# Optimization experiments

Measured on AMD Instinct MI355X. Metric: run time of the kernel, lower is better.

Reference implementation:

```python
import jax, jax.numpy as jnp
import numpy as np

N_NODE = 100000
N_EDGE = 1600000
D_FEAT = 64
DEPTH = 3
BASEALPHA = 1.0


def setup_inputs() -> dict:
    key = jax.random.key(0)
    k1, k2, k3 = jax.random.split(key, 3)
    x = jax.random.normal(k1, (N_NODE, D_FEAT), dtype=jnp.float32)
    edge_index = jax.random.randint(k2, (2, N_EDGE), 0, N_NODE, dtype=jnp.int64)
    edge_attr = jax.random.uniform(k3, (N_EDGE,), dtype=jnp.float32)
    # learnable polynomial coefficients, init = min(1/alpha, 1) = 1.0
    alphas = jnp.ones((DEPTH + 1,), dtype=jnp.float32)
    return {"x": x, "edge_index": edge_index, "edge_attr": edge_attr, "alphas": alphas}


def reference(x, edge_index, edge_attr, alphas):
    n = x.shape[0]
    row, col = edge_index[0], edge_index[1]
    # GCN symmetric degree normalization: val_e = d_row^-1/2 * w_e * d_col^-1/2
    deg = jax.ops.segment_sum(edge_attr, row, num_segments=n)
    safe_deg = jnp.where(deg > 0, deg, 1.0)
    dinv = jnp.where(deg > 0, jax.lax.rsqrt(safe_deg), 0.0)
    val = dinv[row] * edge_attr * dinv[col]  # [E]

    a = BASEALPHA * jnp.tanh(alphas)  # [depth+1]

    def spmm(h):  # (adj @ h): out[i] = sum_{e: row_e=i} val_e * h[col_e]
        return jax.ops.segment_sum(val[:, None] * h[col], row, num_segments=n)

    # PowerConv recurrence: x_0 = x; x_L = a_L * (adj @ x_{L-1})
    xs = [x]
    for L in range(1, DEPTH + 1):
        xs.append(a[L] * spmm(xs[-1]))
    return jnp.stack(xs, axis=1)  # [N, depth+1, d]
```

## Files before the change

kernel.cpp:

```cpp
#include <hip/hip_runtime.h>
#include <math.h>

#define N_NODE 100000
#define N_EDGE 1600000
#define D_FEAT 64
#define DEPTH  3
#define OUT_STRIDE ((DEPTH + 1) * D_FEAT)

#define NB  256
#define RPB 391
#define CAP 8192
#define S1_BS 512
#define S1_CHUNK 8192
#define S1_BLOCKS ((N_EDGE + S1_CHUNK - 1) / S1_CHUNK)

#define NOCT 16
#define OCT_DIV 6250
#define NCELL (RPB * NOCT)
#define NCHUNK (NCELL / 8)

#define DEG_SCALE 33554432.0f

typedef float  f32x4 __attribute__((ext_vector_type(4)));

__device__ __forceinline__ unsigned int bf16_rne(float f) {
    unsigned int u = __float_as_uint(f);
    return (u + 0x7FFFu + ((u >> 16) & 1u)) >> 16;
}

__global__ __launch_bounds__(S1_BS) void stage1_bucket(
        const int* __restrict__ ei, const float* __restrict__ ea,
        int* __restrict__ bucket_cursor, int2* __restrict__ bucket) {
    __shared__ int hist[NB];
    __shared__ int segb[NB];
    int tid = threadIdx.x;
    int e0 = blockIdx.x * S1_CHUNK;

    for (int i = tid; i < NB; i += S1_BS) hist[i] = 0;
    __syncthreads();

    for (int k = 0; k < S1_CHUNK; k += S1_BS) {
        int e = e0 + k + tid;
        if (e < N_EDGE) {
            int r = ei[e];
            atomicAdd(&hist[r / RPB], 1);
        }
    }
    __syncthreads();

    for (int i = tid; i < NB; i += S1_BS) {
        int h = hist[i];
        segb[i] = (h > 0) ? atomicAdd(&bucket_cursor[i], h) : 0;
        hist[i] = 0;
    }
    __syncthreads();

    for (int k = 0; k < S1_CHUNK; k += S1_BS) {
        int e = e0 + k + tid;
        if (e < N_EDGE) {
            int r  = ei[e];
            int b  = r / RPB;
            int rl = r - b * RPB;
            int c  = ei[N_EDGE + e];
            float w = ea[e];
            int lofs = atomicAdd(&hist[b], 1);
            int pos  = segb[b] + lofs;
            if (pos < CAP)
                bucket[(size_t)b * CAP + pos] =
                    make_int2((rl << 17) | c, __float_as_int(w));
        }
    }
}

__global__ void bucket_scan_kernel(const int* __restrict__ bucket_cursor,
                                   int* __restrict__ bucket_base,
                                   const float* __restrict__ alphas,
                                   float* __restrict__ a_vals) {
    __shared__ int sc[NB];
    int tid = threadIdx.x;
    int v = bucket_cursor[tid];
    sc[tid] = v;
    __syncthreads();
    for (int off = 1; off < NB; off <<= 1) {
        int t = (tid >= off) ? sc[tid - off] : 0;
        __syncthreads();
        sc[tid] += t;
        __syncthreads();
    }
    bucket_base[tid] = sc[tid] - v;
    if (tid < DEPTH + 1) a_vals[tid] = tanhf(alphas[tid]);
}

__global__ __launch_bounds__(1024) void stage2_fused(
        const int2* __restrict__ bucket, const int* __restrict__ bucket_cnt,
        const int* __restrict__ bucket_base,
        int* __restrict__ row_ptr, int* __restrict__ row_end,
        float* __restrict__ dinv, int2* __restrict__ csr) {
    __shared__ int          cnt2[NCELL];
    __shared__ unsigned int wdeg[RPB];
    __shared__ int          sc[1024];
    __shared__ int2         staged[CAP];
    int b = blockIdx.x, tid = threadIdx.x;

    for (int i = tid; i < NCELL; i += 1024) cnt2[i] = 0;
    if (tid < RPB) wdeg[tid] = 0u;
    __syncthreads();

    int cnt = bucket_cnt[b];
    const int2* src = bucket + (size_t)b * CAP;

    for (int i = tid; i < cnt; i += 1024) {
        int2 e = src[i];
        int rl = e.x >> 17;
        int c  = e.x & 0x1FFFF;
        int oc = c / OCT_DIV;
        atomicAdd(&cnt2[rl * NOCT + oc], 1);
        atomicAdd(&wdeg[rl],
                  (unsigned int)(__int_as_float(e.y) * DEG_SCALE + 0.5f));
    }
    __syncthreads();

    int lsum = 0;
    if (tid < NCHUNK) {
        int base = tid * 8;
        #pragma unroll
        for (int j = 0; j < 8; ++j) lsum += cnt2[base + j];
    }
    sc[tid] = lsum;
    __syncthreads();
    for (int off = 1; off < 1024; off <<= 1) {
        int t = (tid >= off) ? sc[tid - off] : 0;
        __syncthreads();
        sc[tid] += t;
        __syncthreads();
    }
    if (tid < NCHUNK) {
        int run = sc[tid] - lsum;
        int base = tid * 8;
        #pragma unroll
        for (int j = 0; j < 8; ++j) {
            int v = cnt2[base + j];
            cnt2[base + j] = run;
            run += v;
        }
    }
    __syncthreads();

    int base_b = bucket_base[b];
    if (tid < RPB) {
        int row = b * RPB + tid;
        if (row < N_NODE) {
            int rb = cnt2[tid * NOCT];
            int re = (tid == RPB - 1) ? cnt : cnt2[(tid + 1) * NOCT];
            row_ptr[row] = base_b + rb;
            row_end[row] = base_b + re;
            float d = (float)wdeg[tid] * (1.0f / DEG_SCALE);
            dinv[row] = (d > 0.0f) ? rsqrtf(d) : 0.0f;
        }
    }
    __syncthreads();

    for (int i = tid; i < cnt; i += 1024) {
        int2 e = src[i];
        int rl = e.x >> 17;
        int c  = e.x & 0x1FFFF;
        int oc = c / OCT_DIV;
        int pos = atomicAdd(&cnt2[rl * NOCT + oc], 1);
        staged[pos] = make_int2(c, e.y);
    }
    __syncthreads();

    for (int i = tid; i < cnt; i += 1024) csr[base_b + i] = staged[i];
}

__global__ void init_out_kernel(const float* __restrict__ x,
                                const float* __restrict__ dinv,
                                float* __restrict__ out,
                                unsigned short* __restrict__ hb0,
                                int write_hb) {
    int i = blockIdx.x * blockDim.x + threadIdx.x;
    if (i < N_NODE * (D_FEAT / 4)) {
        int n  = i >> 4;
        int d4 = (i & 15) << 2;
        float4 v = *(const float4*)&x[(size_t)n * D_FEAT + d4];
        f32x4 vv = {v.x, v.y, v.z, v.w};
        __builtin_nontemporal_store(
            vv, (f32x4*)&out[(size_t)n * OUT_STRIDE + d4]);
        if (write_hb) {
            float s = dinv[n];
            uint2 o;
            o.x = bf16_rne(v.x * s) | (bf16_rne(v.y * s) << 16);
            o.y = bf16_rne(v.z * s) | (bf16_rne(v.w * s) << 16);
            *(uint2*)&hb0[(size_t)n * D_FEAT + d4] = o;
        }
    }
}

__global__ __launch_bounds__(256) void spmm_bf16_kernel(
        const int* __restrict__ row_ptr,
        const int* __restrict__ row_end,
        const int2* __restrict__ csr,
        const float* __restrict__ a_vals,
        const float* __restrict__ dinv,
        const unsigned short* __restrict__ hsrc,
        unsigned short* __restrict__ hdst,
        float* __restrict__ out,
        int L, int write_hdst) {
    int node = blockIdx.x * (blockDim.x >> 6) + (threadIdx.x >> 6);
    int lane = threadIdx.x & 63;
    if (node >= N_NODE) return;
    int beg = row_ptr[node];
    int end = row_end[node];
    int g = lane >> 3;
    int q = lane & 7;

    float acc[8] = {0, 0, 0, 0, 0, 0, 0, 0};

    for (int chunk = beg; chunk < end; chunk += 64) {
        int idx = chunk + lane;
        int2 pv = (idx < end) ? csr[idx] : make_int2(0, 0);
        int navail = end - chunk;
        if (navail > 64) navail = 64;
        for (int t = 0; t < navail; t += 8) {
            int sub = t + g;
            int   cc = __shfl(pv.x, sub);
            float vv = __int_as_float(__shfl(pv.y, sub));
            bool valid = (sub < navail);
            int   c_safe = valid ? cc : 0;
            float v_safe = valid ? vv : 0.0f;
            uint4 hv = *(const uint4*)&hsrc[(size_t)c_safe * D_FEAT + (q << 3)];
            acc[0] += v_safe * __uint_as_float((hv.x & 0xFFFFu) << 16);
            acc[1] += v_safe * __uint_as_float(hv.x & 0xFFFF0000u);
            acc[2] += v_safe * __uint_as_float((hv.y & 0xFFFFu) << 16);
            acc[3] += v_safe * __uint_as_float(hv.y & 0xFFFF0000u);
            acc[4] += v_safe * __uint_as_float((hv.z & 0xFFFFu) << 16);
            acc[5] += v_safe * __uint_as_float(hv.z & 0xFFFF0000u);
            acc[6] += v_safe * __uint_as_float((hv.w & 0xFFFFu) << 16);
            acc[7] += v_safe * __uint_as_float(hv.w & 0xFFFF0000u);
        }
    }

    #pragma unroll
    for (int j = 0; j < 8; ++j) {
        acc[j] += __shfl_down(acc[j], 32);
        acc[j] += __shfl_down(acc[j], 16);
        acc[j] += __shfl_down(acc[j], 8);
    }

    if (g == 0) {
        float di = dinv[node];
        float aL = a_vals[L];
        float s1 = aL * di;
        float s2 = s1 * di;
        f32x4 r0 = {s1 * acc[0], s1 * acc[1], s1 * acc[2], s1 * acc[3]};
        f32x4 r1 = {s1 * acc[4], s1 * acc[5], s1 * acc[6], s1 * acc[7]};
        size_t ob = (size_t)node * OUT_STRIDE + L * D_FEAT + (q << 3);
        __builtin_nontemporal_store(r0, (f32x4*)&out[ob]);
        __builtin_nontemporal_store(r1, (f32x4*)&out[ob + 4]);
        if (write_hdst) {
            uint4 o;
            o.x = bf16_rne(s2 * acc[0]) | (bf16_rne(s2 * acc[1]) << 16);
            o.y = bf16_rne(s2 * acc[2]) | (bf16_rne(s2 * acc[3]) << 16);
            o.z = bf16_rne(s2 * acc[4]) | (bf16_rne(s2 * acc[5]) << 16);
            o.w = bf16_rne(s2 * acc[6]) | (bf16_rne(s2 * acc[7]) << 16);
            *(uint4*)&hdst[(size_t)node * D_FEAT + (q << 3)] = o;
        }
    }
}

__global__ void spmm_f32_kernel(const int* __restrict__ row_ptr,
                                const int* __restrict__ row_end,
                                const int2* __restrict__ csr,
                                const float* __restrict__ a_vals,
                                const float* __restrict__ dinv,
                                float* __restrict__ out,
                                int L) {
    int node = blockIdx.x * (blockDim.x >> 6) + (threadIdx.x >> 6);
    int lane = threadIdx.x & 63;
    if (node >= N_NODE) return;
    int beg = row_ptr[node];
    int end = row_end[node];
    int g = lane >> 4;
    int q = lane & 15;
    int src_base = (L - 1) * D_FEAT + (q << 2);

    float4 acc = make_float4(0.0f, 0.0f, 0.0f, 0.0f);
    for (int chunk = beg; chunk < end; chunk += 64) {
        int idx = chunk + lane;
        int2 pv = (idx < end) ? csr[idx] : make_int2(0, 0);
        int navail = end - chunk;
        if (navail > 64) navail = 64;
        for (int t = 0; t < navail; t += 4) {
            int sub = t + g;
            int   cc = __shfl(pv.x, sub);
            float vv = __int_as_float(__shfl(pv.y, sub));
            bool valid = (sub < navail);
            int   c_safe = valid ? cc : 0;
            float v_safe = valid ? (vv * dinv[c_safe]) : 0.0f;
            const float4 hv =
                *(const float4*)&out[(size_t)c_safe * OUT_STRIDE + src_base];
            acc.x += v_safe * hv.x;
            acc.y += v_safe * hv.y;
            acc.z += v_safe * hv.z;
            acc.w += v_safe * hv.w;
        }
    }
    acc.x += __shfl_down(acc.x, 32);
    acc.y += __shfl_down(acc.y, 32);
    acc.z += __shfl_down(acc.z, 32);
    acc.w += __shfl_down(acc.w, 32);
    acc.x += __shfl_down(acc.x, 16);
    acc.y += __shfl_down(acc.y, 16);
    acc.z += __shfl_down(acc.z, 16);
    acc.w += __shfl_down(acc.w, 16);
    if (g == 0) {
        float s1 = a_vals[L] * dinv[node];
        float4 r = make_float4(s1 * acc.x, s1 * acc.y, s1 * acc.z, s1 * acc.w);
        *(float4*)&out[(size_t)node * OUT_STRIDE + L * D_FEAT + (q << 2)] = r;
    }
}

extern "C" void kernel_launch(void* const* d_in, const int* in_sizes, int n_in,
                              void* d_out, int out_size, void* d_ws, size_t ws_size,
                              hipStream_t stream) {
    const float* x      = (const float*)d_in[0];
    const int*   ei     = (const int*)d_in[1];
    const float* ea     = (const float*)d_in[2];
    const float* alphas = (const float*)d_in[3];
    float*       out    = (float*)d_out;

    int2*  csr          = (int2*)d_ws;
    int*   row_ptr      = (int*)(csr + N_EDGE);
    int*   row_end      = row_ptr + N_NODE;
    float* dinv         = (float*)(row_end + N_NODE);
    int*   bucket_cursor= (int*)(dinv + N_NODE);
    int*   bucket_base  = bucket_cursor + NB;
    float* a_vals       = (float*)(bucket_base + NB);
    int2*  bucket       = (int2*)(a_vals + 4);
    unsigned short* hb0 = (unsigned short*)bucket;
    unsigned short* hb1 = hb0 + (size_t)N_NODE * D_FEAT;

    size_t base_bytes = (size_t)((char*)bucket - (char*)d_ws);
    size_t need_bf16  = base_bytes +
        2 * (size_t)N_NODE * D_FEAT * sizeof(unsigned short);
    int use_bf16 = (ws_size >= need_bf16) ? 1 : 0;

    hipMemsetAsync(bucket_cursor, 0, NB * sizeof(int), stream);

    stage1_bucket<<<S1_BLOCKS, S1_BS, 0, stream>>>(ei, ea, bucket_cursor, bucket);
    bucket_scan_kernel<<<1, NB, 0, stream>>>(bucket_cursor, bucket_base,
                                             alphas, a_vals);
    stage2_fused<<<NB, 1024, 0, stream>>>(bucket, bucket_cursor, bucket_base,
                                          row_ptr, row_end, dinv, csr);
    init_out_kernel<<<(N_NODE * (D_FEAT / 4) + 255) / 256, 256, 0, stream>>>(
        x, dinv, out, hb0, use_bf16);

    int nodes_per_block = 256 / 64;
    int spmm_blocks = (N_NODE + nodes_per_block - 1) / nodes_per_block;
    if (use_bf16) {
        spmm_bf16_kernel<<<spmm_blocks, 256, 0, stream>>>(row_ptr, row_end, csr,
            a_vals, dinv, hb0, hb1, out, 1, 1);
        spmm_bf16_kernel<<<spmm_blocks, 256, 0, stream>>>(row_ptr, row_end, csr,
            a_vals, dinv, hb1, hb0, out, 2, 1);
        spmm_bf16_kernel<<<spmm_blocks, 256, 0, stream>>>(row_ptr, row_end, csr,
            a_vals, dinv, hb0, hb1, out, 3, 0);
    } else {
        for (int L = 1; L <= DEPTH; ++L) {
            spmm_f32_kernel<<<spmm_blocks, 256, 0, stream>>>(row_ptr, row_end, csr,
                a_vals, dinv, out, L);
        }
    }
}
```

Before: 331.3 us.

## Split bf16 feature buffer into 16-feature slabs processed in separate passes

The bf16 hidden-state buffer is re-laid out as four slabs of 16 features each, and the SpMM kernel runs one pass per slab, with 16 lanes per node instead of 64. Each pass gathers from a 3.2 MB slab that can stay resident in cache, so random neighbour gathers hit cache instead of HBM. The cost is reading the CSR edge list four times per layer and doing more launch-level work per node. CSR loads are also made nontemporal.

```diff
diff --git a/kernel.cpp b/kernel.cpp
--- a/kernel.cpp
+++ b/kernel.cpp
@@ -18,6 +18,11 @@
 #define OCT_DIV 6250
 #define NCELL (RPB * NOCT)
 #define NCHUNK (NCELL / 8)
+
+#define PASSES 4
+#define FPP    16
+#define NODES_PER_BLOCK 16
+#define BPP (N_NODE / NODES_PER_BLOCK)
 
 #define DEG_SCALE 33554432.0f
 
@@ -188,10 +193,12 @@
             vv, (f32x4*)&out[(size_t)n * OUT_STRIDE + d4]);
         if (write_hb) {
             float s = dinv[n];
+            int pass = d4 >> 4;
+            int fo   = d4 & 15;
             uint2 o;
             o.x = bf16_rne(v.x * s) | (bf16_rne(v.y * s) << 16);
             o.y = bf16_rne(v.z * s) | (bf16_rne(v.w * s) << 16);
-            *(uint2*)&hb0[(size_t)n * D_FEAT + d4] = o;
+            *(uint2*)&hb0[((size_t)pass * N_NODE + n) * FPP + fo] = o;
         }
     }
 }
@@ -206,29 +213,40 @@
         unsigned short* __restrict__ hdst,
         float* __restrict__ out,
         int L, int write_hdst) {
-    int node = blockIdx.x * (blockDim.x >> 6) + (threadIdx.x >> 6);
+    int pass = blockIdx.x / BPP;
+    int nb   = blockIdx.x - pass * BPP;
     int lane = threadIdx.x & 63;
-    if (node >= N_NODE) return;
+    int grp  = lane >> 4;
+    int node = nb * NODES_PER_BLOCK + (threadIdx.x >> 6) * 4 + grp;
+    int l16  = lane & 15;
+    int s    = l16 >> 1;
+    int f    = l16 & 1;
+
     int beg = row_ptr[node];
     int end = row_end[node];
-    int g = lane >> 3;
-    int q = lane & 7;
+
+    const unsigned short* slab = hsrc + (size_t)pass * N_NODE * FPP;
 
     float acc[8] = {0, 0, 0, 0, 0, 0, 0, 0};
 
-    for (int chunk = beg; chunk < end; chunk += 64) {
-        int idx = chunk + lane;
-        int2 pv = (idx < end) ? csr[idx] : make_int2(0, 0);
+    for (int chunk = beg; chunk < end; chunk += 16) {
+        int idx = chunk + l16;
+        int2 pv = make_int2(0, 0);
+        if (idx < end) {
+            long long t =
+                __builtin_nontemporal_load((const long long*)(csr + idx));
+            pv = *(int2*)&t;
+        }
         int navail = end - chunk;
-        if (navail > 64) navail = 64;
+        if (navail > 16) navail = 16;
         for (int t = 0; t < navail; t += 8) {
-            int sub = t + g;
-            int   cc = __shfl(pv.x, sub);
-            float vv = __int_as_float(__shfl(pv.y, sub));
+            int sub = t + s;
+            int   cc = __shfl(pv.x, sub, 16);
+            float vv = __int_as_float(__shfl(pv.y, sub, 16));
             bool valid = (sub < navail);
             int   c_safe = valid ? cc : 0;
             float v_safe = valid ? vv : 0.0f;
-            uint4 hv = *(const uint4*)&hsrc[(size_t)c_safe * D_FEAT + (q << 3)];
+            uint4 hv = *(const uint4*)&slab[(size_t)c_safe * FPP + (f << 3)];
             acc[0] += v_safe * __uint_as_float((hv.x & 0xFFFFu) << 16);
             acc[1] += v_safe * __uint_as_float(hv.x & 0xFFFF0000u);
             acc[2] += v_safe * __uint_as_float((hv.y & 0xFFFFu) << 16);
@@ -242,19 +260,20 @@
 
     #pragma unroll
     for (int j = 0; j < 8; ++j) {
-        acc[j] += __shfl_down(acc[j], 32);
-        acc[j] += __shfl_down(acc[j], 16);
         acc[j] += __shfl_down(acc[j], 8);
-    }
-
-    if (g == 0) {
+        acc[j] += __shfl_down(acc[j], 4);
+        acc[j] += __shfl_down(acc[j], 2);
+    }
+
+    if (l16 < 2) {
         float di = dinv[node];
         float aL = a_vals[L];
         float s1 = aL * di;
         float s2 = s1 * di;
         f32x4 r0 = {s1 * acc[0], s1 * acc[1], s1 * acc[2], s1 * acc[3]};
         f32x4 r1 = {s1 * acc[4], s1 * acc[5], s1 * acc[6], s1 * acc[7]};
-        size_t ob = (size_t)node * OUT_STRIDE + L * D_FEAT + (q << 3);
+        size_t ob = (size_t)node * OUT_STRIDE + L * D_FEAT + pass * FPP
+                  + (f << 3);
         __builtin_nontemporal_store(r0, (f32x4*)&out[ob]);
         __builtin_nontemporal_store(r1, (f32x4*)&out[ob + 4]);
         if (write_hdst) {
@@ -263,7 +282,7 @@
             o.y = bf16_rne(s2 * acc[2]) | (bf16_rne(s2 * acc[3]) << 16);
             o.z = bf16_rne(s2 * acc[4]) | (bf16_rne(s2 * acc[5]) << 16);
             o.w = bf16_rne(s2 * acc[6]) | (bf16_rne(s2 * acc[7]) << 16);
-            *(uint4*)&hdst[(size_t)node * D_FEAT + (q << 3)] = o;
+            *(uint4*)&hdst[((size_t)pass * N_NODE + node) * FPP + (f << 3)] = o;
         }
     }
 }
@@ -355,16 +374,17 @@
     init_out_kernel<<<(N_NODE * (D_FEAT / 4) + 255) / 256, 256, 0, stream>>>(
         x, dinv, out, hb0, use_bf16);
 
-    int nodes_per_block = 256 / 64;
-    int spmm_blocks = (N_NODE + nodes_per_block - 1) / nodes_per_block;
     if (use_bf16) {
-        spmm_bf16_kernel<<<spmm_blocks, 256, 0, stream>>>(row_ptr, row_end, csr,
+        int grid = PASSES * BPP;
+        spmm_bf16_kernel<<<grid, 256, 0, stream>>>(row_ptr, row_end, csr,
             a_vals, dinv, hb0, hb1, out, 1, 1);
-        spmm_bf16_kernel<<<spmm_blocks, 256, 0, stream>>>(row_ptr, row_end, csr,
+        spmm_bf16_kernel<<<grid, 256, 0, stream>>>(row_ptr, row_end, csr,
             a_vals, dinv, hb1, hb0, out, 2, 1);
-        spmm_bf16_kernel<<<spmm_blocks, 256, 0, stream>>>(row_ptr, row_end, csr,
+        spmm_bf16_kernel<<<grid, 256, 0, stream>>>(row_ptr, row_end, csr,
             a_vals, dinv, hb0, hb1, out, 3, 0);
     } else {
+        int nodes_per_block = 256 / 64;
+        int spmm_blocks = (N_NODE + nodes_per_block - 1) / nodes_per_block;
         for (int L = 1; L <= DEPTH; ++L) {
             spmm_f32_kernel<<<spmm_blocks, 256, 0, stream>>>(row_ptr, row_end, csr,
                 a_vals, dinv, out, L);
```

New measurement: 402.8 us. 21.6% more time.

## Map one node per 16-lane group in bf16 SpMM, removing cross-lane reduction

Applied to the files above, without the earlier changes.

The bf16 SpMM kernel now gives each node a 16-lane quarter-wavefront, four nodes per wave, instead of a full 64-lane wave split into 8 edge groups. Each lane owns 4 features and walks the node's edges serially, so the final shuffle reduction goes away and every lane writes output. This raises node-level parallelism and cuts redundant lanes for low-degree rows (about 16 edges per node on average). In exchange each lane does a serial pass over the edges with 8-byte gathers, and offsets use 32-bit arithmetic. The N_NODE bounds check is removed because the grid divides N_NODE exactly.

```diff
diff --git a/kernel.cpp b/kernel.cpp
--- a/kernel.cpp
+++ b/kernel.cpp
@@ -18,6 +18,9 @@
 #define OCT_DIV 6250
 #define NCELL (RPB * NOCT)
 #define NCHUNK (NCELL / 8)
+
+#define SPMM_NPB 16
+#define SPMM_BLOCKS (N_NODE / SPMM_NPB)
 
 #define DEG_SCALE 33554432.0f
 
@@ -206,65 +209,52 @@
         unsigned short* __restrict__ hdst,
         float* __restrict__ out,
         int L, int write_hdst) {
-    int node = blockIdx.x * (blockDim.x >> 6) + (threadIdx.x >> 6);
+    int wid  = threadIdx.x >> 6;
     int lane = threadIdx.x & 63;
-    if (node >= N_NODE) return;
+    int grp  = lane >> 4;
+    int l16  = lane & 15;
+    int node = blockIdx.x * SPMM_NPB + wid * 4 + grp;
+    unsigned int fo = (unsigned int)(l16 << 2);
+
     int beg = row_ptr[node];
     int end = row_end[node];
-    int g = lane >> 3;
-    int q = lane & 7;
-
-    float acc[8] = {0, 0, 0, 0, 0, 0, 0, 0};
-
-    for (int chunk = beg; chunk < end; chunk += 64) {
-        int idx = chunk + lane;
+
+    float acc0 = 0.0f, acc1 = 0.0f, acc2 = 0.0f, acc3 = 0.0f;
+
+    for (int chunk = beg; chunk < end; chunk += 16) {
+        int idx = chunk + l16;
         int2 pv = (idx < end) ? csr[idx] : make_int2(0, 0);
         int navail = end - chunk;
-        if (navail > 64) navail = 64;
-        for (int t = 0; t < navail; t += 8) {
-            int sub = t + g;
-            int   cc = __shfl(pv.x, sub);
-            float vv = __int_as_float(__shfl(pv.y, sub));
-            bool valid = (sub < navail);
-            int   c_safe = valid ? cc : 0;
-            float v_safe = valid ? vv : 0.0f;
-            uint4 hv = *(const uint4*)&hsrc[(size_t)c_safe * D_FEAT + (q << 3)];
-            acc[0] += v_safe * __uint_as_float((hv.x & 0xFFFFu) << 16);
-            acc[1] += v_safe * __uint_as_float(hv.x & 0xFFFF0000u);
-            acc[2] += v_safe * __uint_as_float((hv.y & 0xFFFFu) << 16);
-            acc[3] += v_safe * __uint_as_float(hv.y & 0xFFFF0000u);
-            acc[4] += v_safe * __uint_as_float((hv.z & 0xFFFFu) << 16);
-            acc[5] += v_safe * __uint_as_float(hv.z & 0xFFFF0000u);
-            acc[6] += v_safe * __uint_as_float((hv.w & 0xFFFFu) << 16);
-            acc[7] += v_safe * __uint_as_float(hv.w & 0xFFFF0000u);
-        }
-    }
-
-    #pragma unroll
-    for (int j = 0; j < 8; ++j) {
-        acc[j] += __shfl_down(acc[j], 32);
-        acc[j] += __shfl_down(acc[j], 16);
-        acc[j] += __shfl_down(acc[j], 8);
-    }
-
-    if (g == 0) {
-        float di = dinv[node];
-        float aL = a_vals[L];
-        float s1 = aL * di;
-        float s2 = s1 * di;
-        f32x4 r0 = {s1 * acc[0], s1 * acc[1], s1 * acc[2], s1 * acc[3]};
-        f32x4 r1 = {s1 * acc[4], s1 * acc[5], s1 * acc[6], s1 * acc[7]};
-        size_t ob = (size_t)node * OUT_STRIDE + L * D_FEAT + (q << 3);
-        __builtin_nontemporal_store(r0, (f32x4*)&out[ob]);
-        __builtin_nontemporal_store(r1, (f32x4*)&out[ob + 4]);
-        if (write_hdst) {
-            uint4 o;
-            o.x = bf16_rne(s2 * acc[0]) | (bf16_rne(s2 * acc[1]) << 16);
-            o.y = bf16_rne(s2 * acc[2]) | (bf16_rne(s2 * acc[3]) << 16);
-            o.z = bf16_rne(s2 * acc[4]) | (bf16_rne(s2 * acc[5]) << 16);
-            o.w = bf16_rne(s2 * acc[6]) | (bf16_rne(s2 * acc[7]) << 16);
-            *(uint4*)&hdst[(size_t)node * D_FEAT + (q << 3)] = o;
-        }
+        if (navail > 16) navail = 16;
+        for (int t = 0; t < navail; t += 4) {
+            #pragma unroll
+            for (int k = 0; k < 4; ++k) {
+                int sub = t + k;
+                int   cc = __shfl(pv.x, sub, 16);
+                float vv = __int_as_float(__shfl(pv.y, sub, 16));
+                float w  = (sub < navail) ? vv : 0.0f;
+                unsigned int off = ((unsigned int)cc << 6) + fo;
+                uint2 hv = *(const uint2*)&hsrc[off];
+                acc0 += w * __uint_as_float((hv.x & 0xFFFFu) << 16);
+                acc1 += w * __uint_as_float(hv.x & 0xFFFF0000u);
+                acc2 += w * __uint_as_float((hv.y & 0xFFFFu) << 16);
+                acc3 += w * __uint_as_float(hv.y & 0xFFFF0000u);
+            }
+        }
+    }
+
+    float di = dinv[node];
+    float aL = a_vals[L];
+    float s1 = aL * di;
+    float s2 = s1 * di;
+    f32x4 r = {s1 * acc0, s1 * acc1, s1 * acc2, s1 * acc3};
+    __builtin_nontemporal_store(
+        r, (f32x4*)&out[(size_t)node * OUT_STRIDE + L * D_FEAT + fo]);
+    if (write_hdst) {
+        uint2 o;
+        o.x = bf16_rne(s2 * acc0) | (bf16_rne(s2 * acc1) << 16);
+        o.y = bf16_rne(s2 * acc2) | (bf16_rne(s2 * acc3) << 16);
+        *(uint2*)&hdst[(size_t)node * D_FEAT + fo] = o;
     }
 }
 
@@ -355,16 +345,16 @@
     init_out_kernel<<<(N_NODE * (D_FEAT / 4) + 255) / 256, 256, 0, stream>>>(
         x, dinv, out, hb0, use_bf16);
 
-    int nodes_per_block = 256 / 64;
-    int spmm_blocks = (N_NODE + nodes_per_block - 1) / nodes_per_block;
     if (use_bf16) {
-        spmm_bf16_kernel<<<spmm_blocks, 256, 0, stream>>>(row_ptr, row_end, csr,
+        spmm_bf16_kernel<<<SPMM_BLOCKS, 256, 0, stream>>>(row_ptr, row_end, csr,
             a_vals, dinv, hb0, hb1, out, 1, 1);
-        spmm_bf16_kernel<<<spmm_blocks, 256, 0, stream>>>(row_ptr, row_end, csr,
+        spmm_bf16_kernel<<<SPMM_BLOCKS, 256, 0, stream>>>(row_ptr, row_end, csr,
             a_vals, dinv, hb1, hb0, out, 2, 1);
-        spmm_bf16_kernel<<<spmm_blocks, 256, 0, stream>>>(row_ptr, row_end, csr,
+        spmm_bf16_kernel<<<SPMM_BLOCKS, 256, 0, stream>>>(row_ptr, row_end, csr,
             a_vals, dinv, hb0, hb1, out, 3, 0);
     } else {
+        int nodes_per_block = 256 / 64;
+        int spmm_blocks = (N_NODE + nodes_per_block - 1) / nodes_per_block;
         for (int L = 1; L <= DEPTH; ++L) {
             spmm_f32_kernel<<<spmm_blocks, 256, 0, stream>>>(row_ptr, row_end, csr,
                 a_vals, dinv, out, L);
```

Result: faster. 322.4 us (-2.7%).
